# Kernel optimization log

Hardware: AMD Instinct MI355X
Metric: run time of the kernel (lower is better)

Reference implementation:

```python
import jax, jax.numpy as jnp
import numpy as np

N = 40000      # n_nodes
E = 640000     # n_edges (avg degree 16)
D = 128        # hidden_dim
L = 4          # n_layers
EPS = 1e-6     # equinox RMSNorm default eps


def setup_inputs() -> dict:
    key = jax.random.key(0)
    ks = jax.random.split(key, 11)
    s = 1.0 / np.sqrt(D)
    return {
        "x": jax.random.normal(ks[0], (N, D), jnp.float32),
        "e": jax.random.randint(ks[1], (E, 2), 0, N, dtype=jnp.int32),
        # conv layers (stacked over L, matching eqx.filter_vmap construction)
        "Wc": jax.random.normal(ks[2], (L, D, D), jnp.float32) * s,
        "bc": jax.random.normal(ks[3], (L, D), jnp.float32) * s,
        "gc": jnp.ones((L, D), jnp.float32),   # RMSNorm weight
        "bgc": jnp.zeros((L, D), jnp.float32),  # RMSNorm bias
        # hidden layers
        "Wh": jax.random.normal(ks[4], (L, D, D), jnp.float32) * s,
        "bh": jax.random.normal(ks[5], (L, D), jnp.float32) * s,
        "gh": jnp.ones((L, D), jnp.float32),
        "bgh": jnp.zeros((L, D), jnp.float32),
    }


def _rmsnorm(h, g, b):
    return h * jax.lax.rsqrt(jnp.mean(h * h, axis=-1, keepdims=True) + EPS) * g + b


def reference(x, e, Wc, bc, gc, bgc, Wh, bh, gh, bgh):
    src, dst = e[:, 0], e[:, 1]

    def step(h, params):
        W, b, g, bg, W2, b2, g2, bg2 = params
        # --- GConvLayerEdges ---
        m = jax.nn.relu(jnp.einsum('ed,od->eo', h[src], W) + b)   # [E, D]
        # degree (segment_sum of ones_like(m) in original; all columns equal)
        deg = jax.ops.segment_sum(jnp.ones((E, 1), h.dtype), dst, num_segments=N)
        mm = jax.ops.segment_max(m, dst, num_segments=N)          # [N, D]
        mm = jnp.where(deg == 0, 0.0, mm)
        h = _rmsnorm(h + mm, g, bg)
        # --- HiddenLayer ---
        y = jax.nn.relu(jnp.einsum('nd,od->no', h, W2) + b2)
        h = _rmsnorm(h + y, g2, bg2)
        return h, None

    out, _ = jax.lax.scan(step, x, (Wc, bc, gc, bgc, Wh, bh, gh, bgh))
    return out
```

## Files before the change

kernel.cpp:

```cpp
#include <hip/hip_runtime.h>
#include <hip/hip_bf16.h>
#include <stdint.h>
#include <string.h>

#define NN 40000
#define NE 640000
#define D  128
#define NL 4
#define EPSV 1e-6f

typedef __attribute__((ext_vector_type(8))) short          s16x8;
typedef __attribute__((ext_vector_type(8))) unsigned short u16x8;
typedef __attribute__((ext_vector_type(4))) unsigned short u16x4;
typedef __attribute__((ext_vector_type(4))) float          f32x4;

static __device__ __forceinline__ unsigned short f2b_bits(float f) {
  uint32_t u = __float_as_uint(f);
  uint32_t r = (u + 0x7fffu + ((u >> 16) & 1u)) >> 16;
  return (unsigned short)r;
}
static __device__ __forceinline__ float b2f(unsigned short b) {
  return __uint_as_float((uint32_t)b << 16);
}

__global__ void k_prep(const float* __restrict__ Wc, const float* __restrict__ Wh,
                       unsigned short* __restrict__ wcb, unsigned short* __restrict__ whb) {
  int i = blockIdx.x * 256 + threadIdx.x;
  if (i < NL * D * D) {
    wcb[i] = f2b_bits(Wc[i]);
    whb[i] = f2b_bits(Wh[i]);
  }
}

__global__ void k_count(const int* __restrict__ e, int* __restrict__ deg) {
  int i = blockIdx.x * 256 + threadIdx.x;
  if (i < NE) atomicAdd(&deg[e[2 * i + 1]], 1);
}

__global__ void k_alloc(const int* __restrict__ deg, int* __restrict__ total,
                        int* __restrict__ rs) {
  int i = blockIdx.x * 256 + threadIdx.x;
  if (i < NN) rs[i] = atomicAdd(total, deg[i]);
}

__global__ void k_fill(const int* __restrict__ e, const int* __restrict__ rs,
                       int* __restrict__ cursor, int* __restrict__ csr) {
  int i = blockIdx.x * 256 + threadIdx.x;
  if (i < NE) {
    int s = e[2 * i + 0];
    int d = e[2 * i + 1];
    int p = atomicAdd(&cursor[d], 1);
    csr[rs[d] + p] = s;
  }
}

__global__ __launch_bounds__(256) void k_gemm0(
    const float* __restrict__ hin,
    const unsigned short* __restrict__ Wb,
    const float* __restrict__ bias,
    unsigned short* __restrict__ tout) {
  __shared__ float lds[4][16][D];
  int wave = threadIdx.x >> 6, lane = threadIdx.x & 63;
  int rowbase = (blockIdx.x * 4 + wave) * 16;
  int c15 = lane & 15, grp = lane >> 4;

  s16x8 a[4];
  {
    const float* hp = hin + (size_t)(rowbase + c15) * D;
#pragma unroll
    for (int ks = 0; ks < 4; ++ks) {
      int k0 = ks * 32 + grp * 8;
      f32x4 x0 = *(const f32x4*)(hp + k0);
      f32x4 x1 = *(const f32x4*)(hp + k0 + 4);
      u16x8 av;
      av[0] = f2b_bits(x0[0]); av[1] = f2b_bits(x0[1]);
      av[2] = f2b_bits(x0[2]); av[3] = f2b_bits(x0[3]);
      av[4] = f2b_bits(x1[0]); av[5] = f2b_bits(x1[1]);
      av[6] = f2b_bits(x1[2]); av[7] = f2b_bits(x1[3]);
      a[ks] = __builtin_bit_cast(s16x8, av);
    }
  }

  f32x4 acc[8];
#pragma unroll
  for (int ct = 0; ct < 8; ++ct) { f32x4 z = {0.f, 0.f, 0.f, 0.f}; acc[ct] = z; }
#pragma unroll
  for (int ct = 0; ct < 8; ++ct) {
    const unsigned short* wp = Wb + (size_t)(ct * 16 + c15) * D;
#pragma unroll
    for (int ks = 0; ks < 4; ++ks) {
      s16x8 b = *(const s16x8*)(wp + ks * 32 + grp * 8);
      acc[ct] = __builtin_amdgcn_mfma_f32_16x16x32_bf16(a[ks], b, acc[ct], 0, 0, 0);
    }
  }
#pragma unroll
  for (int ct = 0; ct < 8; ++ct) {
    int col = ct * 16 + c15;
    float bv = bias[col];
#pragma unroll
    for (int r = 0; r < 4; ++r)
      lds[wave][grp * 4 + r][col] = fmaxf(acc[ct][r] + bv, 0.f);
  }
  __syncthreads();
#pragma unroll
  for (int it = 0; it < 4; ++it) {
    int idx = it * 512 + lane * 8;
    int r = idx >> 7, c = idx & 127;
    const float* lp = &lds[wave][r][c];
    f32x4 v0 = *(const f32x4*)lp;
    f32x4 v1 = *(const f32x4*)(lp + 4);
    u16x8 ov;
    ov[0] = f2b_bits(v0[0]); ov[1] = f2b_bits(v0[1]);
    ov[2] = f2b_bits(v0[2]); ov[3] = f2b_bits(v0[3]);
    ov[4] = f2b_bits(v1[0]); ov[5] = f2b_bits(v1[1]);
    ov[6] = f2b_bits(v1[2]); ov[7] = f2b_bits(v1[3]);
    *(u16x8*)(tout + (size_t)(rowbase + r) * D + c) = ov;
  }
}

template <int WRITE_T>
__global__ __launch_bounds__(512) void k_layer(
    const float* __restrict__ hin,
    const uint32_t* __restrict__ tp,
    const int* __restrict__ rs, const int* __restrict__ deg, const int* __restrict__ csr,
    const float* __restrict__ gcv, const float* __restrict__ bgcv,
    const unsigned short* __restrict__ Whb, const float* __restrict__ bhv,
    const float* __restrict__ ghv, const float* __restrict__ bghv,
    const unsigned short* __restrict__ Wcb, const float* __restrict__ bcv,
    float* __restrict__ hout, unsigned short* __restrict__ tout) {
  __shared__ float u[16][132];
  int tid = threadIdx.x;
  int wave = tid >> 6, lane = tid & 63;
  int q = lane & 15, g = lane >> 4;
  int l = lane & 31;
  int hbase = lane & 32;
  int rowbase = blockIdx.x * 16;

  {
    int nl = wave * 2 + (lane >> 5);
    int n = rowbase + nl;
    int r0 = rs[n], dn = deg[n];
    const char* tb = (const char*)tp;
    uint32_t loff = (uint32_t)l * 8u;
    int d0 = l * 4;

    f32x4 hv   = *(const f32x4*)(hin + (size_t)n * D + d0);
    f32x4 gc4  = *(const f32x4*)(gcv + d0);
    f32x4 bgc4 = *(const f32x4*)(bgcv + d0);

    u16x4 ma = {0, 0, 0, 0}, mb = {0, 0, 0, 0};
    int cnt = dn < 32 ? dn : 32;
    int off = (l < cnt) ? l : (cnt - 1);
    int idx = csr[cnt > 0 ? r0 + off : 0];
    int cother = __shfl_xor(cnt, 32);
    int cmax = cnt > cother ? cnt : cother;
    for (int c = 0; c < cmax; c += 8) {
      uint2 p0, p1, p2, p3, p4, p5, p6, p7;
#define GLOAD(k, pv)                                                        \
      {                                                                     \
        int e = c + k; if (e > cnt - 1) e = cnt - 1;                        \
        int sl = e < 0 ? 0 : e;                                             \
        uint32_t s = (uint32_t)__shfl(idx, hbase + sl);                     \
        pv = *(const uint2*)(tb + ((s << 8) + loff));                       \
        if (e < 0) { pv.x = 0u; pv.y = 0u; }                                \
      }
      GLOAD(0, p0) GLOAD(1, p1) GLOAD(2, p2) GLOAD(3, p3)
      GLOAD(4, p4) GLOAD(5, p5) GLOAD(6, p6) GLOAD(7, p7)
#undef GLOAD
      ma = __builtin_elementwise_max(ma, __builtin_bit_cast(u16x4, p0));
      mb = __builtin_elementwise_max(mb, __builtin_bit_cast(u16x4, p1));
      ma = __builtin_elementwise_max(ma, __builtin_bit_cast(u16x4, p2));
      mb = __builtin_elementwise_max(mb, __builtin_bit_cast(u16x4, p3));
      ma = __builtin_elementwise_max(ma, __builtin_bit_cast(u16x4, p4));
      mb = __builtin_elementwise_max(mb, __builtin_bit_cast(u16x4, p5));
      ma = __builtin_elementwise_max(ma, __builtin_bit_cast(u16x4, p6));
      mb = __builtin_elementwise_max(mb, __builtin_bit_cast(u16x4, p7));
    }
    for (int i = r0 + 32; i < r0 + dn; ++i) {
      uint32_t s = (uint32_t)csr[i];
      uint2 p = *(const uint2*)(tb + ((s << 8) + loff));
      ma = __builtin_elementwise_max(ma, __builtin_bit_cast(u16x4, p));
    }
    ma = __builtin_elementwise_max(ma, mb);

    float u0 = hv[0] + b2f(ma[0]);
    float u1 = hv[1] + b2f(ma[1]);
    float u2 = hv[2] + b2f(ma[2]);
    float u3 = hv[3] + b2f(ma[3]);
    float ss = u0 * u0 + u1 * u1 + u2 * u2 + u3 * u3;
#pragma unroll
    for (int off2 = 16; off2; off2 >>= 1) ss += __shfl_xor(ss, off2);
    float rf = rsqrtf(ss * (1.f / D) + EPSV);
    f32x4 o;
    o[0] = u0 * rf * gc4[0] + bgc4[0];
    o[1] = u1 * rf * gc4[1] + bgc4[1];
    o[2] = u2 * rf * gc4[2] + bgc4[2];
    o[3] = u3 * rf * gc4[3] + bgc4[3];
    *(f32x4*)&u[nl][d0] = o;
  }
  __syncthreads();

  const char* whB = (const char*)Whb;
  uint32_t wrow = (uint32_t)(wave * 16 + q) * (D * 2);
  s16x8 a[4];
#pragma unroll
  for (int ks = 0; ks < 4; ++ks) {
    int k0 = ks * 32 + g * 8;
    f32x4 x0 = *(const f32x4*)&u[q][k0];
    f32x4 x1 = *(const f32x4*)&u[q][k0 + 4];
    u16x8 av;
    av[0] = f2b_bits(x0[0]); av[1] = f2b_bits(x0[1]);
    av[2] = f2b_bits(x0[2]); av[3] = f2b_bits(x0[3]);
    av[4] = f2b_bits(x1[0]); av[5] = f2b_bits(x1[1]);
    av[6] = f2b_bits(x1[2]); av[7] = f2b_bits(x1[3]);
    a[ks] = __builtin_bit_cast(s16x8, av);
  }
  f32x4 acc = {0.f, 0.f, 0.f, 0.f};
#pragma unroll
  for (int ks = 0; ks < 4; ++ks) {
    s16x8 b = *(const s16x8*)(whB + wrow + (uint32_t)(ks * 32 + g * 8) * 2);
    acc = __builtin_amdgcn_mfma_f32_16x16x32_bf16(a[ks], b, acc, 0, 0, 0);
  }
  __syncthreads();
  {
    int col = wave * 16 + q;
    float bv = bhv[col];
#pragma unroll
    for (int r = 0; r < 4; ++r)
      u[g * 4 + r][col] += fmaxf(acc[r] + bv, 0.f);
  }
  __syncthreads();
  {
    int d0 = lane * 2;
    float2 gh2  = *(const float2*)(ghv + d0);
    float2 bgh2 = *(const float2*)(bghv + d0);
#pragma unroll
    for (int j = 0; j < 2; ++j) {
      int r = wave * 2 + j;
      float u0 = u[r][d0], u1 = u[r][d0 + 1];
      float ss = u0 * u0 + u1 * u1;
#pragma unroll
      for (int off2 = 32; off2; off2 >>= 1) ss += __shfl_xor(ss, off2);
      float rf = rsqrtf(ss * (1.f / D) + EPSV);
      float o0 = u0 * rf * gh2.x + bgh2.x;
      float o1 = u1 * rf * gh2.y + bgh2.y;
      u[r][d0]     = o0;
      u[r][d0 + 1] = o1;
      float2 o; o.x = o0; o.y = o1;
      *(float2*)(hout + (size_t)(rowbase + r) * D + d0) = o;
    }
  }

  if (WRITE_T) {
    __syncthreads();
    const char* wcB = (const char*)Wcb;
    s16x8 a2[4];
#pragma unroll
    for (int ks = 0; ks < 4; ++ks) {
      int k0 = ks * 32 + g * 8;
      f32x4 x0 = *(const f32x4*)&u[q][k0];
      f32x4 x1 = *(const f32x4*)&u[q][k0 + 4];
      u16x8 av;
      av[0] = f2b_bits(x0[0]); av[1] = f2b_bits(x0[1]);
      av[2] = f2b_bits(x0[2]); av[3] = f2b_bits(x0[3]);
      av[4] = f2b_bits(x1[0]); av[5] = f2b_bits(x1[1]);
      av[6] = f2b_bits(x1[2]); av[7] = f2b_bits(x1[3]);
      a2[ks] = __builtin_bit_cast(s16x8, av);
    }
    f32x4 acc2 = {0.f, 0.f, 0.f, 0.f};
#pragma unroll
    for (int ks = 0; ks < 4; ++ks) {
      s16x8 b = *(const s16x8*)(wcB + wrow + (uint32_t)(ks * 32 + g * 8) * 2);
      acc2 = __builtin_amdgcn_mfma_f32_16x16x32_bf16(a2[ks], b, acc2, 0, 0, 0);
    }
    __syncthreads();
    {
      int col = wave * 16 + q;
      float bv = bcv[col];
#pragma unroll
      for (int r = 0; r < 4; ++r)
        u[g * 4 + r][col] = fmaxf(acc2[r] + bv, 0.f);
    }
    __syncthreads();
    {
      int r = tid >> 5, c = (tid & 31) * 4;
      f32x4 v = *(const f32x4*)&u[r][c];
      u16x4 ov;
      ov[0] = f2b_bits(v[0]); ov[1] = f2b_bits(v[1]);
      ov[2] = f2b_bits(v[2]); ov[3] = f2b_bits(v[3]);
      *(u16x4*)(tout + (size_t)(rowbase + r) * D + c) = ov;
    }
  }
}

extern "C" void kernel_launch(void* const* d_in, const int* in_sizes, int n_in,
                              void* d_out, int out_size, void* d_ws, size_t ws_size,
                              hipStream_t stream) {
  (void)in_sizes; (void)n_in; (void)out_size; (void)ws_size;
  const float* x   = (const float*)d_in[0];
  const int*   e   = (const int*)d_in[1];
  const float* Wc  = (const float*)d_in[2];
  const float* bc  = (const float*)d_in[3];
  const float* gc  = (const float*)d_in[4];
  const float* bgc = (const float*)d_in[5];
  const float* Wh  = (const float*)d_in[6];
  const float* bh  = (const float*)d_in[7];
  const float* gh  = (const float*)d_in[8];
  const float* bgh = (const float*)d_in[9];
  float* out = (float*)d_out;

  char* base = (char*)d_ws;
  unsigned short* t0  = (unsigned short*)(base + 0);
  unsigned short* t1  = (unsigned short*)(base + 10240000);
  float*          hA  = (float*)(base + 20480000);
  unsigned short* wcb = (unsigned short*)(base + 40960000);
  unsigned short* whb = (unsigned short*)(base + 41091072);
  int*            deg = (int*)(base + 41222144);
  int*            cur = (int*)(base + 41382144);
  int*            tot = (int*)(base + 41542144);
  int*            rs  = (int*)(base + 41542208);
  int*            csr = (int*)(base + 41702208);

  k_prep<<<512, 256, 0, stream>>>(Wc, Wh, wcb, whb);
  hipMemsetAsync(deg, 0, 2 * 160000 + 64, stream);
  k_count<<<2500, 256, 0, stream>>>(e, deg);
  k_alloc<<<157, 256, 0, stream>>>(deg, tot, rs);
  k_fill<<<2500, 256, 0, stream>>>(e, rs, cur, csr);

  k_gemm0<<<625, 256, 0, stream>>>(x, wcb, bc, t0);

  unsigned short* tbuf[2] = {t0, t1};
  for (int l = 0; l < NL; ++l) {
    const float* hin = (l == 0) ? x : hA;
    const uint32_t* tin = (const uint32_t*)tbuf[l & 1];
    if (l < NL - 1) {
      k_layer<1><<<2500, 512, 0, stream>>>(
          hin, tin, rs, deg, csr,
          gc + l * D, bgc + l * D,
          whb + (size_t)l * D * D, bh + l * D, gh + l * D, bgh + l * D,
          wcb + (size_t)(l + 1) * D * D, bc + (l + 1) * D,
          hA, tbuf[(l + 1) & 1]);
    } else {
      k_layer<0><<<2500, 512, 0, stream>>>(
          hin, tin, rs, deg, csr,
          gc + l * D, bgc + l * D,
          whb + (size_t)l * D * D, bh + l * D, gh + l * D, bgh + l * D,
          nullptr, nullptr,
          out, nullptr);
    }
  }
}
```

Measured before the change: 259.2 us.

## Pad CSR rows to multiples of eight with sentinel zero row for branchless gather

CSR row allocations are rounded up to multiples of 8, and padding slots are filled with a sentinel node index that points to an all-zero row appended after each message buffer. The aggregation now has each wave handle two nodes across all 64 lanes (2 columns per lane) and reads indices straight from CSR in unrolled groups of 8, with no shuffles, clamping or tail loop. This removes per-edge index broadcast and bounds logic, at the cost of extra padded gathers, a larger CSR, and a new init kernel.

New measurement: 268.3 us. +3.5%, slower.

```diff
diff --git a/kernel.cpp b/kernel.cpp
--- a/kernel.cpp
+++ b/kernel.cpp
@@ -8,10 +8,12 @@
 #define D  128
 #define NL 4
 #define EPSV 1e-6f
+#define CSRP 960000
 
 typedef __attribute__((ext_vector_type(8))) short          s16x8;
 typedef __attribute__((ext_vector_type(8))) unsigned short u16x8;
 typedef __attribute__((ext_vector_type(4))) unsigned short u16x4;
+typedef __attribute__((ext_vector_type(2))) unsigned short u16x2;
 typedef __attribute__((ext_vector_type(4))) float          f32x4;
 
 static __device__ __forceinline__ unsigned short f2b_bits(float f) {
@@ -22,6 +24,9 @@
 static __device__ __forceinline__ float b2f(unsigned short b) {
   return __uint_as_float((uint32_t)b << 16);
 }
+static __device__ __forceinline__ u16x2 pmax(u16x2 x, u16x2 y) {
+  return __builtin_elementwise_max(x, y);
+}
 
 __global__ void k_prep(const float* __restrict__ Wc, const float* __restrict__ Wh,
                        unsigned short* __restrict__ wcb, unsigned short* __restrict__ whb) {
@@ -32,6 +37,13 @@
   }
 }
 
+__global__ void k_init(int* __restrict__ csr, unsigned short* __restrict__ s0,
+                       unsigned short* __restrict__ s1) {
+  int i = blockIdx.x * 256 + threadIdx.x;
+  if (i < CSRP) csr[i] = NN;
+  if (i < D) { s0[i] = 0; s1[i] = 0; }
+}
+
 __global__ void k_count(const int* __restrict__ e, int* __restrict__ deg) {
   int i = blockIdx.x * 256 + threadIdx.x;
   if (i < NE) atomicAdd(&deg[e[2 * i + 1]], 1);
@@ -40,7 +52,7 @@
 __global__ void k_alloc(const int* __restrict__ deg, int* __restrict__ total,
                         int* __restrict__ rs) {
   int i = blockIdx.x * 256 + threadIdx.x;
-  if (i < NN) rs[i] = atomicAdd(total, deg[i]);
+  if (i < NN) rs[i] = atomicAdd(total, (deg[i] + 7) & ~7);
 }
 
 __global__ void k_fill(const int* __restrict__ e, const int* __restrict__ rs,
@@ -132,71 +144,75 @@
   int tid = threadIdx.x;
   int wave = tid >> 6, lane = tid & 63;
   int q = lane & 15, g = lane >> 4;
-  int l = lane & 31;
-  int hbase = lane & 32;
   int rowbase = blockIdx.x * 16;
 
   {
-    int nl = wave * 2 + (lane >> 5);
-    int n = rowbase + nl;
-    int r0 = rs[n], dn = deg[n];
-    const char* tb = (const char*)tp;
-    uint32_t loff = (uint32_t)l * 8u;
-    int d0 = l * 4;
-
-    f32x4 hv   = *(const f32x4*)(hin + (size_t)n * D + d0);
-    f32x4 gc4  = *(const f32x4*)(gcv + d0);
-    f32x4 bgc4 = *(const f32x4*)(bgcv + d0);
-
-    u16x4 ma = {0, 0, 0, 0}, mb = {0, 0, 0, 0};
-    int cnt = dn < 32 ? dn : 32;
-    int off = (l < cnt) ? l : (cnt - 1);
-    int idx = csr[cnt > 0 ? r0 + off : 0];
-    int cother = __shfl_xor(cnt, 32);
-    int cmax = cnt > cother ? cnt : cother;
-    for (int c = 0; c < cmax; c += 8) {
-      uint2 p0, p1, p2, p3, p4, p5, p6, p7;
-#define GLOAD(k, pv)                                                        \
-      {                                                                     \
-        int e = c + k; if (e > cnt - 1) e = cnt - 1;                        \
-        int sl = e < 0 ? 0 : e;                                             \
-        uint32_t s = (uint32_t)__shfl(idx, hbase + sl);                     \
-        pv = *(const uint2*)(tb + ((s << 8) + loff));                       \
-        if (e < 0) { pv.x = 0u; pv.y = 0u; }                                \
-      }
-      GLOAD(0, p0) GLOAD(1, p1) GLOAD(2, p2) GLOAD(3, p3)
-      GLOAD(4, p4) GLOAD(5, p5) GLOAD(6, p6) GLOAD(7, p7)
-#undef GLOAD
-      ma = __builtin_elementwise_max(ma, __builtin_bit_cast(u16x4, p0));
-      mb = __builtin_elementwise_max(mb, __builtin_bit_cast(u16x4, p1));
-      ma = __builtin_elementwise_max(ma, __builtin_bit_cast(u16x4, p2));
-      mb = __builtin_elementwise_max(mb, __builtin_bit_cast(u16x4, p3));
-      ma = __builtin_elementwise_max(ma, __builtin_bit_cast(u16x4, p4));
-      mb = __builtin_elementwise_max(mb, __builtin_bit_cast(u16x4, p5));
-      ma = __builtin_elementwise_max(ma, __builtin_bit_cast(u16x4, p6));
-      mb = __builtin_elementwise_max(mb, __builtin_bit_cast(u16x4, p7));
-    }
-    for (int i = r0 + 32; i < r0 + dn; ++i) {
-      uint32_t s = (uint32_t)csr[i];
-      uint2 p = *(const uint2*)(tb + ((s << 8) + loff));
-      ma = __builtin_elementwise_max(ma, __builtin_bit_cast(u16x4, p));
-    }
-    ma = __builtin_elementwise_max(ma, mb);
-
-    float u0 = hv[0] + b2f(ma[0]);
-    float u1 = hv[1] + b2f(ma[1]);
-    float u2 = hv[2] + b2f(ma[2]);
-    float u3 = hv[3] + b2f(ma[3]);
-    float ss = u0 * u0 + u1 * u1 + u2 * u2 + u3 * u3;
-#pragma unroll
-    for (int off2 = 16; off2; off2 >>= 1) ss += __shfl_xor(ss, off2);
-    float rf = rsqrtf(ss * (1.f / D) + EPSV);
-    f32x4 o;
-    o[0] = u0 * rf * gc4[0] + bgc4[0];
-    o[1] = u1 * rf * gc4[1] + bgc4[1];
-    o[2] = u2 * rf * gc4[2] + bgc4[2];
-    o[3] = u3 * rf * gc4[3] + bgc4[3];
-    *(f32x4*)&u[nl][d0] = o;
+    int waveu = __builtin_amdgcn_readfirstlane(wave);
+    int na = rowbase + waveu * 2;
+    int r0a = rs[na], r0b = rs[na + 1];
+    int dpa = (deg[na] + 7) & ~7;
+    int dpb = (deg[na + 1] + 7) & ~7;
+    const char* __restrict__ tb = (const char*)tp;
+    uint32_t loff = (uint32_t)lane * 4u;
+    int d0 = lane * 2;
+
+    float2 hva  = *(const float2*)(hin + (size_t)na * D + d0);
+    float2 hvb  = *(const float2*)(hin + (size_t)(na + 1) * D + d0);
+    float2 gc2  = *(const float2*)(gcv + d0);
+    float2 bgc2 = *(const float2*)(bgcv + d0);
+
+    const int* __restrict__ csa = csr + r0a;
+    const int* __restrict__ csb = csr + r0b;
+
+#define TL(S) (*(const uint32_t*)((tb + (((uint32_t)(S)) << 8)) + loff))
+    u16x2 a0 = {0,0}, a1 = {0,0}, a2 = {0,0}, a3 = {0,0};
+    for (int i = 0; i < dpa; i += 8) {
+      uint32_t q0 = TL(csa[i+0]), q1 = TL(csa[i+1]), q2 = TL(csa[i+2]), q3 = TL(csa[i+3]);
+      uint32_t q4 = TL(csa[i+4]), q5 = TL(csa[i+5]), q6 = TL(csa[i+6]), q7 = TL(csa[i+7]);
+      a0 = pmax(a0, __builtin_bit_cast(u16x2, q0));
+      a1 = pmax(a1, __builtin_bit_cast(u16x2, q1));
+      a2 = pmax(a2, __builtin_bit_cast(u16x2, q2));
+      a3 = pmax(a3, __builtin_bit_cast(u16x2, q3));
+      a0 = pmax(a0, __builtin_bit_cast(u16x2, q4));
+      a1 = pmax(a1, __builtin_bit_cast(u16x2, q5));
+      a2 = pmax(a2, __builtin_bit_cast(u16x2, q6));
+      a3 = pmax(a3, __builtin_bit_cast(u16x2, q7));
+    }
+    u16x2 b0 = {0,0}, b1 = {0,0}, b2 = {0,0}, b3 = {0,0};
+    for (int i = 0; i < dpb; i += 8) {
+      uint32_t q0 = TL(csb[i+0]), q1 = TL(csb[i+1]), q2 = TL(csb[i+2]), q3 = TL(csb[i+3]);
+      uint32_t q4 = TL(csb[i+4]), q5 = TL(csb[i+5]), q6 = TL(csb[i+6]), q7 = TL(csb[i+7]);
+      b0 = pmax(b0, __builtin_bit_cast(u16x2, q0));
+      b1 = pmax(b1, __builtin_bit_cast(u16x2, q1));
+      b2 = pmax(b2, __builtin_bit_cast(u16x2, q2));
+      b3 = pmax(b3, __builtin_bit_cast(u16x2, q3));
+      b0 = pmax(b0, __builtin_bit_cast(u16x2, q4));
+      b1 = pmax(b1, __builtin_bit_cast(u16x2, q5));
+      b2 = pmax(b2, __builtin_bit_cast(u16x2, q6));
+      b3 = pmax(b3, __builtin_bit_cast(u16x2, q7));
+    }
+#undef TL
+    u16x2 am = pmax(pmax(a0, a1), pmax(a2, a3));
+    u16x2 bm = pmax(pmax(b0, b1), pmax(b2, b3));
+
+    float ua0 = hva.x + b2f(am[0]);
+    float ua1 = hva.y + b2f(am[1]);
+    float ub0 = hvb.x + b2f(bm[0]);
+    float ub1 = hvb.y + b2f(bm[1]);
+    float ssa = ua0 * ua0 + ua1 * ua1;
+    float ssb = ub0 * ub0 + ub1 * ub1;
+#pragma unroll
+    for (int off = 32; off; off >>= 1) {
+      ssa += __shfl_xor(ssa, off);
+      ssb += __shfl_xor(ssb, off);
+    }
+    float rfa = rsqrtf(ssa * (1.f / D) + EPSV);
+    float rfb = rsqrtf(ssb * (1.f / D) + EPSV);
+    int nla = waveu * 2;
+    u[nla][d0]         = ua0 * rfa * gc2.x + bgc2.x;
+    u[nla][d0 + 1]     = ua1 * rfa * gc2.y + bgc2.y;
+    u[nla + 1][d0]     = ub0 * rfb * gc2.x + bgc2.x;
+    u[nla + 1][d0 + 1] = ub1 * rfb * gc2.y + bgc2.y;
   }
   __syncthreads();
 
@@ -311,18 +327,19 @@
 
   char* base = (char*)d_ws;
   unsigned short* t0  = (unsigned short*)(base + 0);
-  unsigned short* t1  = (unsigned short*)(base + 10240000);
-  float*          hA  = (float*)(base + 20480000);
-  unsigned short* wcb = (unsigned short*)(base + 40960000);
-  unsigned short* whb = (unsigned short*)(base + 41091072);
-  int*            deg = (int*)(base + 41222144);
-  int*            cur = (int*)(base + 41382144);
-  int*            tot = (int*)(base + 41542144);
-  int*            rs  = (int*)(base + 41542208);
-  int*            csr = (int*)(base + 41702208);
+  unsigned short* t1  = (unsigned short*)(base + 10240512);
+  float*          hA  = (float*)(base + 20481024);
+  unsigned short* wcb = (unsigned short*)(base + 40961024);
+  unsigned short* whb = (unsigned short*)(base + 41092096);
+  int*            deg = (int*)(base + 41223168);
+  int*            cur = (int*)(base + 41383168);
+  int*            tot = (int*)(base + 41543168);
+  int*            rs  = (int*)(base + 41543232);
+  int*            csr = (int*)(base + 41703232);
 
   k_prep<<<512, 256, 0, stream>>>(Wc, Wh, wcb, whb);
   hipMemsetAsync(deg, 0, 2 * 160000 + 64, stream);
+  k_init<<<3750, 256, 0, stream>>>(csr, t0 + (size_t)NN * D, t1 + (size_t)NN * D);
   k_count<<<2500, 256, 0, stream>>>(e, deg);
   k_alloc<<<157, 256, 0, stream>>>(deg, tot, rs);
   k_fill<<<2500, 256, 0, stream>>>(e, rs, cur, csr);
```
